# Performance work log

Measured on AMD Instinct MI355X. Metric: run time of the kernel, lower is better.

## Reference

```python
import jax, jax.numpy as jnp
import numpy as np

DIM = 1024


def setup_inputs() -> dict:
    key = jax.random.key(0)
    ks = jax.random.split(key, 10)
    B, S, D = 4, 2048, DIM
    std = 1.0 / np.sqrt(D)  # torch Linear default uniform bound
    return {
        "query": jax.random.normal(ks[0], (B, S, D), jnp.float32),
        "key": jax.random.normal(ks[1], (B, S, D), jnp.float32),
        "value": jax.random.normal(ks[2], (B, S, D), jnp.float32),
        "context": jnp.zeros((D,), jnp.float32),
        "Wq": jax.random.uniform(ks[3], (D, D), jnp.float32, -std, std),
        "bq": jax.random.uniform(ks[4], (D,), jnp.float32, -std, std),
        "Wk": jax.random.uniform(ks[5], (D, D), jnp.float32, -std, std),
        "bk": jax.random.uniform(ks[6], (D,), jnp.float32, -std, std),
        "Wv": jax.random.uniform(ks[7], (D, D), jnp.float32, -std, std),
        "bv": jax.random.uniform(ks[8], (D,), jnp.float32, -std, std),
    }


def reference(query, key, value, context, Wq, bq, Wk, bk, Wv, bv):
    scale = query.shape[-1] ** -0.5
    # torch Linear: x @ W.T + b
    q = (query + context) @ Wq.T + bq          # [B,S,D]
    k = (key + context) @ Wk.T + bk            # [B,S,D]
    v = value @ Wv.T + bv                      # [B,S,D]
    scores = jnp.einsum("bqd,bkd->bqk", q, k) * scale  # [B,S,S]
    weights = jax.nn.softmax(scores, axis=-1)
    return jnp.einsum("bqk,bkd->bqd", weights, v)
```

## Files before the change

kernel.cpp:

```cpp
#include <hip/hip_runtime.h>

typedef __attribute__((ext_vector_type(8))) short bf16x8;
typedef __attribute__((ext_vector_type(4))) float floatx4;

constexpr int BATCH = 4;
constexpr int SEQ   = 2048;
constexpr int DIMN  = 1024;
constexpr int M1    = BATCH * SEQ;

__device__ __forceinline__ short f2bf(float f) {
    union { float f; unsigned u; } x; x.f = f;
    unsigned r = x.u + 0x7fffu + ((x.u >> 16) & 1u);
    return (short)(r >> 16);
}
__device__ __forceinline__ float bf2f(short s) {
    union { unsigned u; float f; } x; x.u = ((unsigned)(unsigned short)s) << 16;
    return x.f;
}

__device__ __forceinline__ void async16(const void* g, void* l) {
    __builtin_amdgcn_global_load_lds(
        (const __attribute__((address_space(1))) unsigned int*)g,
        (__attribute__((address_space(3))) unsigned int*)l, 16, 0, 0);
}

#define WAITVM(N) asm volatile("s_waitcnt vmcnt(" #N ")" ::: "memory")
#define MEMFENCE  asm volatile("" ::: "memory")
#define BAR()     __builtin_amdgcn_s_barrier()
#define PRIO(x)   __builtin_amdgcn_s_setprio(x)

template<bool OUT_BF16, int WM>
__device__ __forceinline__ void gemm_core(
    const short* __restrict__ Ab, int lda,
    const short* __restrict__ Bb, int ldb,
    void* __restrict__ Cb, int ldc,
    const float* __restrict__ bias, int K, float scale,
    int m0, int n0)
{
    constexpr int ACH  = WM / 2;
    constexpr int ABY  = WM * 4096;
    constexpr int BUFB = ABY + 32768;
    __shared__ alignas(16) char smem[2][BUFB];
    char* lds = &smem[0][0];

    const int t    = threadIdx.x;
    const int lane = t & 63;
    const int wave = t >> 6;
    const int wr   = wave >> 2;
    const int wc   = wave & 3;
    const int lr   = lane & 15;
    const int lq   = lane >> 4;

    const int srow = t >> 3;
    const int scol = (((t & 7) * 16) ^ (((t >> 3) & 7) << 4)) >> 1;
    const short* pa = Ab + (size_t)(m0 + srow) * lda + scol;
    const short* pb = Bb + (size_t)(n0 + srow) * ldb + scol;
    const size_t rsa = (size_t)64 * lda;
    const size_t rsb = (size_t)64 * ldb;
    const int ldst = t * 16;

    const int roA0 = (wr * (WM * 16) + lr) * 128;
    const int roB0 = ABY + (wc * 64 + lr) * 128;
    const int cp0  = (lq << 4) ^ ((lane & 7) << 4);

    floatx4 acc[WM][4];
    #pragma unroll
    for (int m = 0; m < WM; ++m)
        #pragma unroll
        for (int n = 0; n < 4; ++n) acc[m][n] = (floatx4)(0.f);

    auto stA = [&](int dstb) {
        #pragma unroll
        for (int c = 0; c < ACH; ++c)
            async16(pa + (size_t)c * rsa, lds + dstb + c * 8192 + ldst);
        pa += 64;
    };
    auto stB01 = [&](int dstb) {
        async16(pb,       lds + dstb + ABY +        ldst);
        async16(pb + rsb, lds + dstb + ABY + 8192 + ldst);
    };
    auto stB23 = [&](int dstb) {
        async16(pb + 2 * rsb, lds + dstb + ABY + 16384 + ldst);
        async16(pb + 3 * rsb, lds + dstb + ABY + 24576 + ldst);
        pb += 64;
    };

    const int NT = K >> 6;

    stA(0); stB01(0); stB23(0); stA(BUFB);
    if constexpr (WM == 8) WAITVM(4); else WAITVM(2);
    BAR();

    for (int tt = 0; tt < NT; tt += 2) {
        #pragma unroll
        for (int half = 0; half < 2; ++half) {
            const int bufb = half ? BUFB : 0;
            const int tc   = tt + half;
            const char* rb = lds + bufb;

            if constexpr (WM == 8) {
                bf16x8 af[8], bq_[4];
                #pragma unroll
                for (int m = 0; m < 8; ++m)
                    af[m] = *(const bf16x8*)(rb + roA0 + m * 2048 + cp0);
                bq_[0] = *(const bf16x8*)(rb + roB0 +        cp0);
                bq_[1] = *(const bf16x8*)(rb + roB0 + 2048 + cp0);
                if (tc + 1 < NT) stB01(bufb ^ BUFB);
                BAR(); MEMFENCE;
                PRIO(1);
                #pragma unroll
                for (int m = 0; m < 8; ++m) {
                    acc[m][0] = __builtin_amdgcn_mfma_f32_16x16x32_bf16(af[m], bq_[0], acc[m][0], 0, 0, 0);
                    acc[m][1] = __builtin_amdgcn_mfma_f32_16x16x32_bf16(af[m], bq_[1], acc[m][1], 0, 0, 0);
                }
                PRIO(0);
                MEMFENCE; BAR();
                bq_[2] = *(const bf16x8*)(rb + roB0 + 2 * 2048 + cp0);
                bq_[3] = *(const bf16x8*)(rb + roB0 + 3 * 2048 + cp0);
                if (tc + 1 < NT) stB23(bufb ^ BUFB);
                BAR(); MEMFENCE;
                PRIO(1);
                #pragma unroll
                for (int m = 0; m < 8; ++m) {
                    acc[m][2] = __builtin_amdgcn_mfma_f32_16x16x32_bf16(af[m], bq_[2], acc[m][2], 0, 0, 0);
                    acc[m][3] = __builtin_amdgcn_mfma_f32_16x16x32_bf16(af[m], bq_[3], acc[m][3], 0, 0, 0);
                }
                PRIO(0);
                MEMFENCE; BAR();
                #pragma unroll
                for (int m = 0; m < 8; ++m)
                    af[m] = *(const bf16x8*)(rb + roA0 + m * 2048 + (cp0 ^ 64));
                bq_[0] = *(const bf16x8*)(rb + roB0 +        (cp0 ^ 64));
                bq_[1] = *(const bf16x8*)(rb + roB0 + 2048 + (cp0 ^ 64));
                BAR(); MEMFENCE;
                PRIO(1);
                #pragma unroll
                for (int m = 0; m < 8; ++m) {
                    acc[m][0] = __builtin_amdgcn_mfma_f32_16x16x32_bf16(af[m], bq_[0], acc[m][0], 0, 0, 0);
                    acc[m][1] = __builtin_amdgcn_mfma_f32_16x16x32_bf16(af[m], bq_[1], acc[m][1], 0, 0, 0);
                }
                PRIO(0);
                MEMFENCE; BAR();
                bq_[2] = *(const bf16x8*)(rb + roB0 + 2 * 2048 + (cp0 ^ 64));
                bq_[3] = *(const bf16x8*)(rb + roB0 + 3 * 2048 + (cp0 ^ 64));
                if (tc + 2 < NT) stA(bufb);
                BAR(); MEMFENCE;
                PRIO(1);
                #pragma unroll
                for (int m = 0; m < 8; ++m) {
                    acc[m][2] = __builtin_amdgcn_mfma_f32_16x16x32_bf16(af[m], bq_[2], acc[m][2], 0, 0, 0);
                    acc[m][3] = __builtin_amdgcn_mfma_f32_16x16x32_bf16(af[m], bq_[3], acc[m][3], 0, 0, 0);
                }
                PRIO(0);
                MEMFENCE;
                if (tc + 2 < NT)      { WAITVM(4); }
                else if (tc + 1 < NT) { WAITVM(0); }
                BAR();
            } else {
                bf16x8 af[4][2], bq_[2][2];
                #pragma unroll
                for (int m = 0; m < 4; ++m) {
                    af[m][0] = *(const bf16x8*)(rb + roA0 + m * 2048 + cp0);
                    af[m][1] = *(const bf16x8*)(rb + roA0 + m * 2048 + (cp0 ^ 64));
                }
                #pragma unroll
                for (int n = 0; n < 2; ++n) {
                    bq_[n][0] = *(const bf16x8*)(rb + roB0 + n * 2048 + cp0);
                    bq_[n][1] = *(const bf16x8*)(rb + roB0 + n * 2048 + (cp0 ^ 64));
                }
                if (tc + 1 < NT) { stB01(bufb ^ BUFB); stB23(bufb ^ BUFB); }
                BAR(); MEMFENCE;
                PRIO(1);
                #pragma unroll
                for (int m = 0; m < 4; ++m)
                    #pragma unroll
                    for (int n = 0; n < 2; ++n) {
                        acc[m][n] = __builtin_amdgcn_mfma_f32_16x16x32_bf16(af[m][0], bq_[n][0], acc[m][n], 0, 0, 0);
                        acc[m][n] = __builtin_amdgcn_mfma_f32_16x16x32_bf16(af[m][1], bq_[n][1], acc[m][n], 0, 0, 0);
                    }
                PRIO(0);
                MEMFENCE; BAR();
                #pragma unroll
                for (int n = 0; n < 2; ++n) {
                    bq_[n][0] = *(const bf16x8*)(rb + roB0 + (n + 2) * 2048 + cp0);
                    bq_[n][1] = *(const bf16x8*)(rb + roB0 + (n + 2) * 2048 + (cp0 ^ 64));
                }
                if (tc + 2 < NT) stA(bufb);
                BAR(); MEMFENCE;
                PRIO(1);
                #pragma unroll
                for (int m = 0; m < 4; ++m)
                    #pragma unroll
                    for (int n = 0; n < 2; ++n) {
                        acc[m][n + 2] = __builtin_amdgcn_mfma_f32_16x16x32_bf16(af[m][0], bq_[n][0], acc[m][n + 2], 0, 0, 0);
                        acc[m][n + 2] = __builtin_amdgcn_mfma_f32_16x16x32_bf16(af[m][1], bq_[n][1], acc[m][n + 2], 0, 0, 0);
                    }
                PRIO(0);
                MEMFENCE;
                if (tc + 2 < NT)      { WAITVM(2); }
                else if (tc + 1 < NT) { WAITVM(0); }
                BAR();
            }
        }
    }

    #pragma unroll
    for (int n = 0; n < 4; ++n) {
        const int gn = n0 + wc * 64 + n * 16 + lr;
        const float bv = bias ? bias[gn] : 0.f;
        #pragma unroll
        for (int m = 0; m < WM; ++m) {
            #pragma unroll
            for (int r = 0; r < 4; ++r) {
                const int gm = m0 + wr * (WM * 16) + m * 16 + lq * 4 + r;
                const float v = acc[m][n][r] * scale + bv;
                if (OUT_BF16) ((short*)Cb)[(size_t)gm * ldc + gn] = f2bf(v);
                else          ((float*)Cb)[(size_t)gm * ldc + gn] = v;
            }
        }
    }
}

__global__ __launch_bounds__(512, 2)
void proj_qkv(const short* __restrict__ xq, const short* __restrict__ xk,
              const short* __restrict__ xv,
              const short* __restrict__ Wq_, const short* __restrict__ Wk_,
              const short* __restrict__ Wv_,
              const float* __restrict__ bq_, const float* __restrict__ bk_,
              const float* __restrict__ bv_,
              short* __restrict__ q, short* __restrict__ k, short* __restrict__ vp)
{
    const int b   = blockIdx.x;
    const int xcd = b & 7;
    const int i   = b >> 3;
    const int z   = i >> 5;
    const int r   = i & 31;
    const int mm  = r >> 2;
    const int nn  = r & 3;
    const short* X = (z == 0) ? xq : (z == 1) ? xk : xv;
    const short* W = (z == 0) ? Wq_ : (z == 1) ? Wk_ : Wv_;
    const float* bb = (z == 0) ? bq_ : (z == 1) ? bk_ : bv_;
    short* O = (z == 0) ? q : (z == 1) ? k : vp;
    gemm_core<true, 4>(X, DIMN, W, DIMN, (void*)O, DIMN, bb, DIMN, 1.f,
                       (xcd * 8 + mm) * 128, nn * 256);
}

__global__ __launch_bounds__(512, 2)
void gemm_scores(const short* __restrict__ q, const short* __restrict__ k,
                 short* __restrict__ S, float scale)
{
    const int b   = blockIdx.x;
    const int xcd = b & 7;
    const int i   = b >> 3;
    const int bz  = xcd >> 1;
    const int mh  = xcd & 1;
    const int mm  = i >> 3;
    const int nn  = i & 7;
    gemm_core<true, 8>(q + (size_t)bz * SEQ * DIMN, DIMN,
                       k + (size_t)bz * SEQ * DIMN, DIMN,
                       (void*)(S + (size_t)bz * SEQ * SEQ), SEQ,
                       nullptr, DIMN, scale,
                       (mh * 4 + mm) * 256, nn * 256);
}

__global__ __launch_bounds__(512, 2)
void gemm_pv(const short* __restrict__ P, const short* __restrict__ vt,
             float* __restrict__ O)
{
    const int b   = blockIdx.x;
    const int xcd = b & 7;
    const int i   = b >> 3;
    const int bz  = xcd >> 1;
    const int mh  = xcd & 1;
    const int mm  = i >> 2;
    const int nn  = i & 3;
    gemm_core<false, 4>(P  + (size_t)bz * SEQ * SEQ,  SEQ,
                        vt + (size_t)bz * DIMN * SEQ, SEQ,
                        (void*)(O + (size_t)bz * SEQ * DIMN), DIMN,
                        nullptr, SEQ, 1.f,
                        (mh * 8 + mm) * 128, nn * 256);
}

__global__ __launch_bounds__(256)
void cvt_tri(const float* __restrict__ in0, short* __restrict__ out0,
             const float* __restrict__ in1, short* __restrict__ out1,
             const float* __restrict__ in2, short* __restrict__ out2, int n8)
{
    const int z = blockIdx.z;
    const float* in = (z == 0) ? in0 : (z == 1) ? in1 : in2;
    short* out      = (z == 0) ? out0 : (z == 1) ? out1 : out2;
    const int i = blockIdx.x * 256 + threadIdx.x;
    if (i >= n8) return;
    const float4 a0 = ((const float4*)in)[(size_t)i * 2];
    const float4 a1 = ((const float4*)in)[(size_t)i * 2 + 1];
    const float v[8] = {a0.x, a0.y, a0.z, a0.w, a1.x, a1.y, a1.z, a1.w};
    bf16x8 o;
    #pragma unroll
    for (int j = 0; j < 8; ++j) o[j] = f2bf(v[j]);
    *(bf16x8*)(out + (size_t)i * 8) = o;
}

__global__ __launch_bounds__(256)
void bias3(const float* __restrict__ Wq, const float* __restrict__ Wk,
           const float* __restrict__ Wv,
           const float* __restrict__ bq, const float* __restrict__ bk,
           const float* __restrict__ bv,
           const float* __restrict__ ctx,
           float* __restrict__ oq, float* __restrict__ ok, float* __restrict__ ov)
{
    const int z = blockIdx.y;
    const float* W = (z == 0) ? Wq : (z == 1) ? Wk : Wv;
    const float* b = (z == 0) ? bq : (z == 1) ? bk : bv;
    float*       o = (z == 0) ? oq : (z == 1) ? ok : ov;
    const int n    = blockIdx.x * 4 + (threadIdx.x >> 6);
    const int lane = threadIdx.x & 63;
    float s = 0.f;
    if (z < 2) {
        const float* row = W + (size_t)n * DIMN;
        for (int k = lane * 4; k < DIMN; k += 256) {
            const float4 x = *(const float4*)(row + k);
            const float4 c = *(const float4*)(ctx + k);
            s += x.x * c.x + x.y * c.y + x.z * c.z + x.w * c.w;
        }
        #pragma unroll
        for (int off = 32; off > 0; off >>= 1) s += __shfl_xor(s, off);
    }
    if (lane == 0) o[n] = b[n] + s;
}

__global__ __launch_bounds__(256)
void transpose_v(const short* __restrict__ in, short* __restrict__ out)
{
    __shared__ short t[64][68];
    const int b  = blockIdx.z;
    const int d0 = blockIdx.x * 64;
    const int s0 = blockIdx.y * 64;
    const int r  = threadIdx.x >> 3;
    const int c  = (threadIdx.x & 7) * 8;
    #pragma unroll
    for (int h = 0; h < 2; ++h) {
        const int s = r + h * 32;
        bf16x8 v = *(const bf16x8*)(in + ((size_t)b * SEQ + s0 + s) * DIMN + d0 + c);
        #pragma unroll
        for (int j = 0; j < 8; ++j) t[c + j][s] = v[j];
    }
    __syncthreads();
    #pragma unroll
    for (int h = 0; h < 2; ++h) {
        const int d = r + h * 32;
        bf16x8 v;
        #pragma unroll
        for (int j = 0; j < 8; ++j) v[j] = t[d][c + j];
        *(bf16x8*)(out + ((size_t)b * DIMN + d0 + d) * SEQ + s0 + c) = v;
    }
}

__global__ __launch_bounds__(256)
void softmax_kernel(short* __restrict__ P)
{
    const int bid = blockIdx.x;
    const int xcd = bid & 7;
    const int i   = bid >> 3;
    const int row = (xcd >> 1) * SEQ + (xcd & 1) * 1024 + i;
    short* p = P + (size_t)row * SEQ;
    const int t    = threadIdx.x;
    const int lane = t & 63;
    const int wave = t >> 6;
    __shared__ float red[8];

    bf16x8 raw = *(const bf16x8*)(p + t * 8);
    float v[8];
    float mx = -1e30f;
    #pragma unroll
    for (int j = 0; j < 8; ++j) { v[j] = bf2f(raw[j]); mx = fmaxf(mx, v[j]); }
    #pragma unroll
    for (int off = 32; off > 0; off >>= 1) mx = fmaxf(mx, __shfl_xor(mx, off));
    if (lane == 0) red[wave] = mx;
    __syncthreads();
    mx = fmaxf(fmaxf(red[0], red[1]), fmaxf(red[2], red[3]));

    float e[8], s = 0.f;
    #pragma unroll
    for (int j = 0; j < 8; ++j) { e[j] = __expf(v[j] - mx); s += e[j]; }
    #pragma unroll
    for (int off = 32; off > 0; off >>= 1) s += __shfl_xor(s, off);
    if (lane == 0) red[4 + wave] = s;
    __syncthreads();
    s = red[4] + red[5] + red[6] + red[7];
    const float inv = 1.f / s;

    bf16x8 o;
    #pragma unroll
    for (int j = 0; j < 8; ++j) o[j] = f2bf(e[j] * inv);
    *(bf16x8*)(p + t * 8) = o;
}

extern "C" void kernel_launch(void* const* d_in, const int* in_sizes, int n_in,
                              void* d_out, int out_size, void* d_ws, size_t ws_size,
                              hipStream_t stream)
{
    const float* query = (const float*)d_in[0];
    const float* key_  = (const float*)d_in[1];
    const float* value = (const float*)d_in[2];
    const float* ctx   = (const float*)d_in[3];
    const float* Wq    = (const float*)d_in[4];
    const float* bq    = (const float*)d_in[5];
    const float* Wk    = (const float*)d_in[6];
    const float* bk    = (const float*)d_in[7];
    const float* Wv    = (const float*)d_in[8];
    const float* bv    = (const float*)d_in[9];

    char* ws = (char*)d_ws;
    char* od = (char*)d_out;
    const size_t MB = 1ull << 20;
    short* xq   = (short*)(ws);
    short* xk   = (short*)(ws + 16 * MB);
    short* q_b  = (short*)(ws + 32 * MB);
    short* k_b  = (short*)(ws + 48 * MB);
    short* Wq_b = (short*)(ws + 64 * MB);
    short* Wk_b = (short*)(ws + 66 * MB);
    short* Wv_b = (short*)(ws + 68 * MB);
    float* bq_e = (float*)(ws + 70 * MB);
    float* bk_e = (float*)(ws + 70 * MB + 4096);
    float* bv_e = (float*)(ws + 70 * MB + 8192);
    short* S_b  = (short*)(ws);
    short* v_t  = (short*)(ws + 64 * MB);
    short* xv   = (short*)(od);
    short* vp   = (short*)(od + 16 * MB);

    dim3 blk(256);
    dim3 blk512(512);
    const int W8 = DIMN * DIMN / 8;
    const int X8 = M1 * DIMN / 8;

    cvt_tri<<<dim3(W8 / 256, 1, 3), blk, 0, stream>>>(Wq, Wq_b, Wk, Wk_b, Wv, Wv_b, W8);
    bias3<<<dim3(DIMN / 4, 3), blk, 0, stream>>>(Wq, Wk, Wv, bq, bk, bv, ctx,
                                                 bq_e, bk_e, bv_e);
    cvt_tri<<<dim3(X8 / 256, 1, 3), blk, 0, stream>>>(query, xq, key_, xk, value, xv, X8);

    proj_qkv<<<dim3(768), blk512, 0, stream>>>(xq, xk, xv, Wq_b, Wk_b, Wv_b,
                                               bq_e, bk_e, bv_e, q_b, k_b, vp);
    transpose_v<<<dim3(DIMN / 64, SEQ / 64, BATCH), blk, 0, stream>>>(vp, v_t);

    const float scale = 1.0f / 32.0f;
    gemm_scores<<<dim3(256), blk512, 0, stream>>>(q_b, k_b, S_b, scale);

    softmax_kernel<<<dim3(M1), blk, 0, stream>>>(S_b);

    gemm_pv<<<dim3(256), blk512, 0, stream>>>(S_b, v_t, (float*)d_out);
}
```

Measured before the change: 304.3 us.

## Fuse fp32-to-bf16 input conversion into projection GEMM and restructure score GEMM pipeline

Drops the separate cvt_tri pass over query/key/value. The projection GEMM now loads fp32 activations into registers, converts them to bf16 and writes them into swizzled LDS itself, which removes a full read-write round trip of three 32 MB inputs. The scores GEMM gets a new four-phase single-tile loop that stages A and B in quarters across the MFMA phases. The PV GEMM is split out into its own simplified core. The risk is more register pressure and VALU conversion work inside the projection mainloop, plus a different overlap pattern in the scores kernel.

```diff
diff --git a/kernel.cpp b/kernel.cpp
--- a/kernel.cpp
+++ b/kernel.cpp
@@ -1,6 +1,7 @@
 #include <hip/hip_runtime.h>
 
 typedef __attribute__((ext_vector_type(8))) short bf16x8;
+typedef __attribute__((ext_vector_type(4))) short short4v;
 typedef __attribute__((ext_vector_type(4))) float floatx4;
 
 constexpr int BATCH = 4;
@@ -25,23 +26,21 @@
 }
 
 #define WAITVM(N) asm volatile("s_waitcnt vmcnt(" #N ")" ::: "memory")
-#define MEMFENCE  asm volatile("" ::: "memory")
+#define LGKM0     asm volatile("s_waitcnt lgkmcnt(0)" ::: "memory")
 #define BAR()     __builtin_amdgcn_s_barrier()
 #define PRIO(x)   __builtin_amdgcn_s_setprio(x)
 
-template<bool OUT_BF16, int WM>
-__device__ __forceinline__ void gemm_core(
+template<bool OUT_BF16>
+__device__ __forceinline__ void gemm4ph(
     const short* __restrict__ Ab, int lda,
     const short* __restrict__ Bb, int ldb,
     void* __restrict__ Cb, int ldc,
     const float* __restrict__ bias, int K, float scale,
     int m0, int n0)
 {
-    constexpr int ACH  = WM / 2;
-    constexpr int ABY  = WM * 4096;
-    constexpr int BUFB = ABY + 32768;
-    __shared__ alignas(16) char smem[2][BUFB];
-    char* lds = &smem[0][0];
+    constexpr int BUFB = 65536;
+    __shared__ alignas(16) char smem[2 * BUFB];
+    char* lds = smem;
 
     const int t    = threadIdx.x;
     const int lane = t & 63;
@@ -51,6 +50,306 @@
     const int lr   = lane & 15;
     const int lq   = lane >> 4;
 
+    const int srow  = t >> 3;
+    const int scolB = ((t & 7) * 16) ^ ((srow & 7) << 4);
+    const short* pa = Ab + (size_t)(m0 + srow) * lda + (scolB >> 1);
+    const short* pb = Bb + (size_t)(n0 + srow) * ldb + (scolB >> 1);
+    const size_t rsa = (size_t)64 * lda;
+    const size_t rsb = (size_t)64 * ldb;
+    const int ldst = t * 16;
+
+    const int roA = (wr * 128 + lr) * 128;
+    const int roB = 32768 + (wc * 64 + lr) * 128;
+    const int cs  = (lane & 7) << 4;
+    const int cp0 = (lq << 4) ^ cs;
+    const int cp1 = (64 | (lq << 4)) ^ cs;
+
+    floatx4 acc[8][4];
+    #pragma unroll
+    for (int m = 0; m < 8; ++m)
+        #pragma unroll
+        for (int n = 0; n < 4; ++n) acc[m][n] = (floatx4)(0.f);
+
+    auto stA01 = [&](int d) {
+        async16(pa,       lds + d +        ldst);
+        async16(pa + rsa, lds + d + 8192 + ldst);
+    };
+    auto stA23 = [&](int d) {
+        async16(pa + 2 * rsa, lds + d + 16384 + ldst);
+        async16(pa + 3 * rsa, lds + d + 24576 + ldst);
+        pa += 64;
+    };
+    auto stB01 = [&](int d) {
+        async16(pb,       lds + d + 32768 + ldst);
+        async16(pb + rsb, lds + d + 40960 + ldst);
+    };
+    auto stB23 = [&](int d) {
+        async16(pb + 2 * rsb, lds + d + 49152 + ldst);
+        async16(pb + 3 * rsb, lds + d + 57344 + ldst);
+        pb += 64;
+    };
+
+    const int NT = K >> 6;
+
+    stA01(0); stA23(0); stB01(0); stB23(0);
+    WAITVM(0);
+    BAR();
+
+    int bu = 0;
+    for (int tt = 0; tt < NT; ++tt) {
+        const bool stg = tt + 1 < NT;
+        const int  ob  = bu ^ BUFB;
+        const char* rb = lds + bu;
+        bf16x8 af[4], bq_[4];
+
+        if (stg) stA01(ob);
+        #pragma unroll
+        for (int m = 0; m < 4; ++m) af[m]  = *(const bf16x8*)(rb + roA + m * 2048 + cp0);
+        #pragma unroll
+        for (int n = 0; n < 4; ++n) bq_[n] = *(const bf16x8*)(rb + roB + n * 2048 + cp0);
+        BAR();
+        PRIO(1);
+        #pragma unroll
+        for (int m = 0; m < 4; ++m)
+            #pragma unroll
+            for (int n = 0; n < 4; ++n)
+                acc[m][n] = __builtin_amdgcn_mfma_f32_16x16x32_bf16(af[m], bq_[n], acc[m][n], 0, 0, 0);
+        PRIO(0);
+        BAR();
+
+        if (stg) stA23(ob);
+        #pragma unroll
+        for (int m = 0; m < 4; ++m) af[m] = *(const bf16x8*)(rb + roA + (m + 4) * 2048 + cp0);
+        BAR();
+        PRIO(1);
+        #pragma unroll
+        for (int m = 0; m < 4; ++m)
+            #pragma unroll
+            for (int n = 0; n < 4; ++n)
+                acc[m + 4][n] = __builtin_amdgcn_mfma_f32_16x16x32_bf16(af[m], bq_[n], acc[m + 4][n], 0, 0, 0);
+        PRIO(0);
+        BAR();
+
+        if (stg) stB01(ob);
+        #pragma unroll
+        for (int m = 0; m < 4; ++m) af[m]  = *(const bf16x8*)(rb + roA + m * 2048 + cp1);
+        #pragma unroll
+        for (int n = 0; n < 4; ++n) bq_[n] = *(const bf16x8*)(rb + roB + n * 2048 + cp1);
+        BAR();
+        PRIO(1);
+        #pragma unroll
+        for (int m = 0; m < 4; ++m)
+            #pragma unroll
+            for (int n = 0; n < 4; ++n)
+                acc[m][n] = __builtin_amdgcn_mfma_f32_16x16x32_bf16(af[m], bq_[n], acc[m][n], 0, 0, 0);
+        PRIO(0);
+        BAR();
+
+        if (stg) stB23(ob);
+        #pragma unroll
+        for (int m = 0; m < 4; ++m) af[m] = *(const bf16x8*)(rb + roA + (m + 4) * 2048 + cp1);
+        BAR();
+        PRIO(1);
+        #pragma unroll
+        for (int m = 0; m < 4; ++m)
+            #pragma unroll
+            for (int n = 0; n < 4; ++n)
+                acc[m + 4][n] = __builtin_amdgcn_mfma_f32_16x16x32_bf16(af[m], bq_[n], acc[m + 4][n], 0, 0, 0);
+        PRIO(0);
+        WAITVM(0);
+        BAR();
+        bu = ob;
+    }
+
+    #pragma unroll
+    for (int n = 0; n < 4; ++n) {
+        const int gn = n0 + wc * 64 + n * 16 + lr;
+        const float bv = bias ? bias[gn] : 0.f;
+        #pragma unroll
+        for (int m = 0; m < 8; ++m) {
+            #pragma unroll
+            for (int r = 0; r < 4; ++r) {
+                const int gm = m0 + wr * 128 + m * 16 + lq * 4 + r;
+                const float v = acc[m][n][r] * scale + bv;
+                if (OUT_BF16) ((short*)Cb)[(size_t)gm * ldc + gn] = f2bf(v);
+                else          ((float*)Cb)[(size_t)gm * ldc + gn] = v;
+            }
+        }
+    }
+}
+
+__device__ __forceinline__ void proj_core(
+    const float* __restrict__ Af, int lda,
+    const short* __restrict__ Bb, int ldb,
+    short* __restrict__ Cb, int ldc,
+    const float* __restrict__ bias, int K,
+    int m0, int n0)
+{
+    constexpr int ABY  = 16384;
+    constexpr int BUFB = ABY + 32768;
+    __shared__ alignas(16) char smem[2 * BUFB];
+    char* lds = smem;
+
+    const int t    = threadIdx.x;
+    const int lane = t & 63;
+    const int wave = t >> 6;
+    const int wr   = wave >> 2;
+    const int wc   = wave & 3;
+    const int lr   = lane & 15;
+    const int lq   = lane >> 4;
+
+    const int srow  = t >> 3;
+    const int scolB = ((t & 7) * 16) ^ ((srow & 7) << 4);
+    const short* pb = Bb + (size_t)(n0 + srow) * ldb + (scolB >> 1);
+    const size_t rsb = (size_t)64 * ldb;
+    const int ldst = t * 16;
+
+    const float* pafb = Af + (size_t)(m0 + (t >> 4)) * lda + (t & 15) * 4;
+    const size_t opstr = (size_t)32 * lda;
+    int dwA[4];
+    #pragma unroll
+    for (int o = 0; o < 4; ++o) {
+        const int row = o * 32 + (t >> 4);
+        dwA[o] = row * 128 + (((t & 15) * 8) ^ ((row & 7) << 4));
+    }
+
+    const int roA = (wr * 64 + lr) * 128;
+    const int roB = ABY + (wc * 64 + lr) * 128;
+    const int cs  = (lane & 7) << 4;
+    const int cp0 = (lq << 4) ^ cs;
+    const int cp1 = (64 | (lq << 4)) ^ cs;
+
+    floatx4 acc[4][4];
+    #pragma unroll
+    for (int m = 0; m < 4; ++m)
+        #pragma unroll
+        for (int n = 0; n < 4; ++n) acc[m][n] = (floatx4)(0.f);
+
+    auto stB01 = [&](int d) {
+        async16(pb,       lds + d + ABY +        ldst);
+        async16(pb + rsb, lds + d + ABY + 8192 + ldst);
+    };
+    auto stB23 = [&](int d) {
+        async16(pb + 2 * rsb, lds + d + ABY + 16384 + ldst);
+        async16(pb + 3 * rsb, lds + d + ABY + 24576 + ldst);
+        pb += 64;
+    };
+    float4 rA[4];
+    auto loadA = [&]() {
+        #pragma unroll
+        for (int o = 0; o < 4; ++o)
+            rA[o] = *(const float4*)(pafb + (size_t)o * opstr);
+        pafb += 64;
+    };
+    auto writeA = [&](int d) {
+        #pragma unroll
+        for (int o = 0; o < 4; ++o) {
+            short4v pk;
+            pk[0] = f2bf(rA[o].x); pk[1] = f2bf(rA[o].y);
+            pk[2] = f2bf(rA[o].z); pk[3] = f2bf(rA[o].w);
+            *(short4v*)(lds + d + dwA[o]) = pk;
+        }
+    };
+
+    const int NT = K >> 6;
+
+    loadA();
+    stB01(0); stB23(0);
+    WAITVM(4);
+    writeA(0);
+    LGKM0;
+    WAITVM(0);
+    BAR();
+
+    int bu = 0;
+    for (int tt = 0; tt < NT; ++tt) {
+        const bool stg = tt + 1 < NT;
+        const int  ob  = bu ^ BUFB;
+        const char* rb = lds + bu;
+        bf16x8 af[4][2], bq_[2][2];
+
+        if (stg) { loadA(); stB01(ob); stB23(ob); }
+        #pragma unroll
+        for (int m = 0; m < 4; ++m) {
+            af[m][0] = *(const bf16x8*)(rb + roA + m * 2048 + cp0);
+            af[m][1] = *(const bf16x8*)(rb + roA + m * 2048 + cp1);
+        }
+        #pragma unroll
+        for (int n = 0; n < 2; ++n) {
+            bq_[n][0] = *(const bf16x8*)(rb + roB + n * 2048 + cp0);
+            bq_[n][1] = *(const bf16x8*)(rb + roB + n * 2048 + cp1);
+        }
+        BAR();
+        PRIO(1);
+        #pragma unroll
+        for (int m = 0; m < 4; ++m)
+            #pragma unroll
+            for (int n = 0; n < 2; ++n) {
+                acc[m][n] = __builtin_amdgcn_mfma_f32_16x16x32_bf16(af[m][0], bq_[n][0], acc[m][n], 0, 0, 0);
+                acc[m][n] = __builtin_amdgcn_mfma_f32_16x16x32_bf16(af[m][1], bq_[n][1], acc[m][n], 0, 0, 0);
+            }
+        PRIO(0);
+        BAR();
+
+        #pragma unroll
+        for (int n = 0; n < 2; ++n) {
+            bq_[n][0] = *(const bf16x8*)(rb + roB + (n + 2) * 2048 + cp0);
+            bq_[n][1] = *(const bf16x8*)(rb + roB + (n + 2) * 2048 + cp1);
+        }
+        if (stg) {
+            WAITVM(4);
+            writeA(ob);
+        }
+        BAR();
+        PRIO(1);
+        #pragma unroll
+        for (int m = 0; m < 4; ++m)
+            #pragma unroll
+            for (int n = 0; n < 2; ++n) {
+                acc[m][n + 2] = __builtin_amdgcn_mfma_f32_16x16x32_bf16(af[m][0], bq_[n][0], acc[m][n + 2], 0, 0, 0);
+                acc[m][n + 2] = __builtin_amdgcn_mfma_f32_16x16x32_bf16(af[m][1], bq_[n][1], acc[m][n + 2], 0, 0, 0);
+            }
+        PRIO(0);
+        LGKM0;
+        WAITVM(0);
+        BAR();
+        bu = ob;
+    }
+
+    #pragma unroll
+    for (int n = 0; n < 4; ++n) {
+        const int gn = n0 + wc * 64 + n * 16 + lr;
+        const float bv = bias[gn];
+        #pragma unroll
+        for (int m = 0; m < 4; ++m) {
+            #pragma unroll
+            for (int r = 0; r < 4; ++r) {
+                const int gm = m0 + wr * 64 + m * 16 + lq * 4 + r;
+                Cb[(size_t)gm * ldc + gn] = f2bf(acc[m][n][r] + bv);
+            }
+        }
+    }
+}
+
+__device__ __forceinline__ void gemm_pv_core(
+    const short* __restrict__ Ab, int lda,
+    const short* __restrict__ Bb, int ldb,
+    float* __restrict__ Cb, int ldc, int K,
+    int m0, int n0)
+{
+    constexpr int ABY  = 16384;
+    constexpr int BUFB = ABY + 32768;
+    __shared__ alignas(16) char smem[2][BUFB];
+    char* lds = &smem[0][0];
+
+    const int t    = threadIdx.x;
+    const int lane = t & 63;
+    const int wave = t >> 6;
+    const int wr   = wave >> 2;
+    const int wc   = wave & 3;
+    const int lr   = lane & 15;
+    const int lq   = lane >> 4;
+
     const int srow = t >> 3;
     const int scol = (((t & 7) * 16) ^ (((t >> 3) & 7) << 4)) >> 1;
     const short* pa = Ab + (size_t)(m0 + srow) * lda + scol;
@@ -59,20 +358,19 @@
     const size_t rsb = (size_t)64 * ldb;
     const int ldst = t * 16;
 
-    const int roA0 = (wr * (WM * 16) + lr) * 128;
+    const int roA0 = (wr * 64 + lr) * 128;
     const int roB0 = ABY + (wc * 64 + lr) * 128;
     const int cp0  = (lq << 4) ^ ((lane & 7) << 4);
 
-    floatx4 acc[WM][4];
-    #pragma unroll
-    for (int m = 0; m < WM; ++m)
+    floatx4 acc[4][4];
+    #pragma unroll
+    for (int m = 0; m < 4; ++m)
         #pragma unroll
         for (int n = 0; n < 4; ++n) acc[m][n] = (floatx4)(0.f);
 
     auto stA = [&](int dstb) {
-        #pragma unroll
-        for (int c = 0; c < ACH; ++c)
-            async16(pa + (size_t)c * rsa, lds + dstb + c * 8192 + ldst);
+        async16(pa,       lds + dstb +        ldst);
+        async16(pa + rsa, lds + dstb + 8192 + ldst);
         pa += 64;
     };
     auto stB01 = [&](int dstb) {
@@ -86,144 +384,75 @@
     };
 
     const int NT = K >> 6;
-
     stA(0); stB01(0); stB23(0); stA(BUFB);
-    if constexpr (WM == 8) WAITVM(4); else WAITVM(2);
+    WAITVM(2);
     BAR();
 
-    for (int tt = 0; tt < NT; tt += 2) {
-        #pragma unroll
-        for (int half = 0; half < 2; ++half) {
-            const int bufb = half ? BUFB : 0;
-            const int tc   = tt + half;
-            const char* rb = lds + bufb;
-
-            if constexpr (WM == 8) {
-                bf16x8 af[8], bq_[4];
-                #pragma unroll
-                for (int m = 0; m < 8; ++m)
-                    af[m] = *(const bf16x8*)(rb + roA0 + m * 2048 + cp0);
-                bq_[0] = *(const bf16x8*)(rb + roB0 +        cp0);
-                bq_[1] = *(const bf16x8*)(rb + roB0 + 2048 + cp0);
-                if (tc + 1 < NT) stB01(bufb ^ BUFB);
-                BAR(); MEMFENCE;
-                PRIO(1);
-                #pragma unroll
-                for (int m = 0; m < 8; ++m) {
-                    acc[m][0] = __builtin_amdgcn_mfma_f32_16x16x32_bf16(af[m], bq_[0], acc[m][0], 0, 0, 0);
-                    acc[m][1] = __builtin_amdgcn_mfma_f32_16x16x32_bf16(af[m], bq_[1], acc[m][1], 0, 0, 0);
-                }
-                PRIO(0);
-                MEMFENCE; BAR();
-                bq_[2] = *(const bf16x8*)(rb + roB0 + 2 * 2048 + cp0);
-                bq_[3] = *(const bf16x8*)(rb + roB0 + 3 * 2048 + cp0);
-                if (tc + 1 < NT) stB23(bufb ^ BUFB);
-                BAR(); MEMFENCE;
-                PRIO(1);
-                #pragma unroll
-                for (int m = 0; m < 8; ++m) {
-                    acc[m][2] = __builtin_amdgcn_mfma_f32_16x16x32_bf16(af[m], bq_[2], acc[m][2], 0, 0, 0);
-                    acc[m][3] = __builtin_amdgcn_mfma_f32_16x16x32_bf16(af[m], bq_[3], acc[m][3], 0, 0, 0);
-                }
-                PRIO(0);
-                MEMFENCE; BAR();
-                #pragma unroll
-                for (int m = 0; m < 8; ++m)
-                    af[m] = *(const bf16x8*)(rb + roA0 + m * 2048 + (cp0 ^ 64));
-                bq_[0] = *(const bf16x8*)(rb + roB0 +        (cp0 ^ 64));
-                bq_[1] = *(const bf16x8*)(rb + roB0 + 2048 + (cp0 ^ 64));
-                BAR(); MEMFENCE;
-                PRIO(1);
-                #pragma unroll
-                for (int m = 0; m < 8; ++m) {
-                    acc[m][0] = __builtin_amdgcn_mfma_f32_16x16x32_bf16(af[m], bq_[0], acc[m][0], 0, 0, 0);
-                    acc[m][1] = __builtin_amdgcn_mfma_f32_16x16x32_bf16(af[m], bq_[1], acc[m][1], 0, 0, 0);
-                }
-                PRIO(0);
-                MEMFENCE; BAR();
-                bq_[2] = *(const bf16x8*)(rb + roB0 + 2 * 2048 + (cp0 ^ 64));
-                bq_[3] = *(const bf16x8*)(rb + roB0 + 3 * 2048 + (cp0 ^ 64));
-                if (tc + 2 < NT) stA(bufb);
-                BAR(); MEMFENCE;
-                PRIO(1);
-                #pragma unroll
-                for (int m = 0; m < 8; ++m) {
-                    acc[m][2] = __builtin_amdgcn_mfma_f32_16x16x32_bf16(af[m], bq_[2], acc[m][2], 0, 0, 0);
-                    acc[m][3] = __builtin_amdgcn_mfma_f32_16x16x32_bf16(af[m], bq_[3], acc[m][3], 0, 0, 0);
-                }
-                PRIO(0);
-                MEMFENCE;
-                if (tc + 2 < NT)      { WAITVM(4); }
-                else if (tc + 1 < NT) { WAITVM(0); }
-                BAR();
-            } else {
-                bf16x8 af[4][2], bq_[2][2];
-                #pragma unroll
-                for (int m = 0; m < 4; ++m) {
-                    af[m][0] = *(const bf16x8*)(rb + roA0 + m * 2048 + cp0);
-                    af[m][1] = *(const bf16x8*)(rb + roA0 + m * 2048 + (cp0 ^ 64));
-                }
-                #pragma unroll
-                for (int n = 0; n < 2; ++n) {
-                    bq_[n][0] = *(const bf16x8*)(rb + roB0 + n * 2048 + cp0);
-                    bq_[n][1] = *(const bf16x8*)(rb + roB0 + n * 2048 + (cp0 ^ 64));
-                }
-                if (tc + 1 < NT) { stB01(bufb ^ BUFB); stB23(bufb ^ BUFB); }
-                BAR(); MEMFENCE;
-                PRIO(1);
-                #pragma unroll
-                for (int m = 0; m < 4; ++m)
-                    #pragma unroll
-                    for (int n = 0; n < 2; ++n) {
-                        acc[m][n] = __builtin_amdgcn_mfma_f32_16x16x32_bf16(af[m][0], bq_[n][0], acc[m][n], 0, 0, 0);
-                        acc[m][n] = __builtin_amdgcn_mfma_f32_16x16x32_bf16(af[m][1], bq_[n][1], acc[m][n], 0, 0, 0);
-                    }
-                PRIO(0);
-                MEMFENCE; BAR();
-                #pragma unroll
-                for (int n = 0; n < 2; ++n) {
-                    bq_[n][0] = *(const bf16x8*)(rb + roB0 + (n + 2) * 2048 + cp0);
-                    bq_[n][1] = *(const bf16x8*)(rb + roB0 + (n + 2) * 2048 + (cp0 ^ 64));
-                }
-                if (tc + 2 < NT) stA(bufb);
-                BAR(); MEMFENCE;
-                PRIO(1);
-                #pragma unroll
-                for (int m = 0; m < 4; ++m)
-                    #pragma unroll
-                    for (int n = 0; n < 2; ++n) {
-                        acc[m][n + 2] = __builtin_amdgcn_mfma_f32_16x16x32_bf16(af[m][0], bq_[n][0], acc[m][n + 2], 0, 0, 0);
-                        acc[m][n + 2] = __builtin_amdgcn_mfma_f32_16x16x32_bf16(af[m][1], bq_[n][1], acc[m][n + 2], 0, 0, 0);
-                    }
-                PRIO(0);
-                MEMFENCE;
-                if (tc + 2 < NT)      { WAITVM(2); }
-                else if (tc + 1 < NT) { WAITVM(0); }
-                BAR();
+    int bufb = 0;
+    for (int tc = 0; tc < NT; ++tc) {
+        const char* rb = lds + bufb;
+        bf16x8 af[4][2], bq_[2][2];
+        #pragma unroll
+        for (int m = 0; m < 4; ++m) {
+            af[m][0] = *(const bf16x8*)(rb + roA0 + m * 2048 + cp0);
+            af[m][1] = *(const bf16x8*)(rb + roA0 + m * 2048 + (cp0 ^ 64));
+        }
+        #pragma unroll
+        for (int n = 0; n < 2; ++n) {
+            bq_[n][0] = *(const bf16x8*)(rb + roB0 + n * 2048 + cp0);
+            bq_[n][1] = *(const bf16x8*)(rb + roB0 + n * 2048 + (cp0 ^ 64));
+        }
+        if (tc + 1 < NT) { stB01(bufb ^ BUFB); stB23(bufb ^ BUFB); }
+        BAR();
+        PRIO(1);
+        #pragma unroll
+        for (int m = 0; m < 4; ++m)
+            #pragma unroll
+            for (int n = 0; n < 2; ++n) {
+                acc[m][n] = __builtin_amdgcn_mfma_f32_16x16x32_bf16(af[m][0], bq_[n][0], acc[m][n], 0, 0, 0);
+                acc[m][n] = __builtin_amdgcn_mfma_f32_16x16x32_bf16(af[m][1], bq_[n][1], acc[m][n], 0, 0, 0);
             }
-        }
+        PRIO(0);
+        BAR();
+        #pragma unroll
+        for (int n = 0; n < 2; ++n) {
+            bq_[n][0] = *(const bf16x8*)(rb + roB0 + (n + 2) * 2048 + cp0);
+            bq_[n][1] = *(const bf16x8*)(rb + roB0 + (n + 2) * 2048 + (cp0 ^ 64));
+        }
+        if (tc + 2 < NT) stA(bufb);
+        BAR();
+        PRIO(1);
+        #pragma unroll
+        for (int m = 0; m < 4; ++m)
+            #pragma unroll
+            for (int n = 0; n < 2; ++n) {
+                acc[m][n + 2] = __builtin_amdgcn_mfma_f32_16x16x32_bf16(af[m][0], bq_[n][0], acc[m][n + 2], 0, 0, 0);
+                acc[m][n + 2] = __builtin_amdgcn_mfma_f32_16x16x32_bf16(af[m][1], bq_[n][1], acc[m][n + 2], 0, 0, 0);
+            }
+        PRIO(0);
+        if (tc + 2 < NT)      { WAITVM(2); }
+        else if (tc + 1 < NT) { WAITVM(0); }
+        BAR();
+        bufb ^= BUFB;
     }
 
     #pragma unroll
     for (int n = 0; n < 4; ++n) {
         const int gn = n0 + wc * 64 + n * 16 + lr;
-        const float bv = bias ? bias[gn] : 0.f;
-        #pragma unroll
-        for (int m = 0; m < WM; ++m) {
+        #pragma unroll
+        for (int m = 0; m < 4; ++m) {
             #pragma unroll
             for (int r = 0; r < 4; ++r) {
-                const int gm = m0 + wr * (WM * 16) + m * 16 + lq * 4 + r;
-                const float v = acc[m][n][r] * scale + bv;
-                if (OUT_BF16) ((short*)Cb)[(size_t)gm * ldc + gn] = f2bf(v);
-                else          ((float*)Cb)[(size_t)gm * ldc + gn] = v;
+                const int gm = m0 + wr * 64 + m * 16 + lq * 4 + r;
+                Cb[(size_t)gm * ldc + gn] = acc[m][n][r];
             }
         }
     }
 }
 
 __global__ __launch_bounds__(512, 2)
-void proj_qkv(const short* __restrict__ xq, const short* __restrict__ xk,
-              const short* __restrict__ xv,
+void proj_qkv(const float* __restrict__ xq, const float* __restrict__ xk,
+              const float* __restrict__ xv,
               const short* __restrict__ Wq_, const short* __restrict__ Wk_,
               const short* __restrict__ Wv_,
               const float* __restrict__ bq_, const float* __restrict__ bk_,
@@ -237,12 +466,12 @@
     const int r   = i & 31;
     const int mm  = r >> 2;
     const int nn  = r & 3;
-    const short* X = (z == 0) ? xq : (z == 1) ? xk : xv;
+    const float* X = (z == 0) ? xq : (z == 1) ? xk : xv;
     const short* W = (z == 0) ? Wq_ : (z == 1) ? Wk_ : Wv_;
     const float* bb = (z == 0) ? bq_ : (z == 1) ? bk_ : bv_;
     short* O = (z == 0) ? q : (z == 1) ? k : vp;
-    gemm_core<true, 4>(X, DIMN, W, DIMN, (void*)O, DIMN, bb, DIMN, 1.f,
-                       (xcd * 8 + mm) * 128, nn * 256);
+    proj_core(X, DIMN, W, DIMN, O, DIMN, bb, DIMN,
+              (xcd * 8 + mm) * 128, nn * 256);
 }
 
 __global__ __launch_bounds__(512, 2)
@@ -256,11 +485,11 @@
     const int mh  = xcd & 1;
     const int mm  = i >> 3;
     const int nn  = i & 7;
-    gemm_core<true, 8>(q + (size_t)bz * SEQ * DIMN, DIMN,
-                       k + (size_t)bz * SEQ * DIMN, DIMN,
-                       (void*)(S + (size_t)bz * SEQ * SEQ), SEQ,
-                       nullptr, DIMN, scale,
-                       (mh * 4 + mm) * 256, nn * 256);
+    gemm4ph<true>(q + (size_t)bz * SEQ * DIMN, DIMN,
+                  k + (size_t)bz * SEQ * DIMN, DIMN,
+                  (void*)(S + (size_t)bz * SEQ * SEQ), SEQ,
+                  nullptr, DIMN, scale,
+                  (mh * 4 + mm) * 256, nn * 256);
 }
 
 __global__ __launch_bounds__(512, 2)
@@ -274,11 +503,10 @@
     const int mh  = xcd & 1;
     const int mm  = i >> 2;
     const int nn  = i & 3;
-    gemm_core<false, 4>(P  + (size_t)bz * SEQ * SEQ,  SEQ,
-                        vt + (size_t)bz * DIMN * SEQ, SEQ,
-                        (void*)(O + (size_t)bz * SEQ * DIMN), DIMN,
-                        nullptr, SEQ, 1.f,
-                        (mh * 8 + mm) * 128, nn * 256);
+    gemm_pv_core(P  + (size_t)bz * SEQ * SEQ,  SEQ,
+                 vt + (size_t)bz * DIMN * SEQ, SEQ,
+                 O + (size_t)bz * SEQ * DIMN, DIMN, SEQ,
+                 (mh * 8 + mm) * 128, nn * 256);
 }
 
 __global__ __launch_bounds__(256)
@@ -411,10 +639,8 @@
     const float* bv    = (const float*)d_in[9];
 
     char* ws = (char*)d_ws;
-    char* od = (char*)d_out;
     const size_t MB = 1ull << 20;
-    short* xq   = (short*)(ws);
-    short* xk   = (short*)(ws + 16 * MB);
+    short* vp   = (short*)(ws);
     short* q_b  = (short*)(ws + 32 * MB);
     short* k_b  = (short*)(ws + 48 * MB);
     short* Wq_b = (short*)(ws + 64 * MB);
@@ -425,20 +651,17 @@
     float* bv_e = (float*)(ws + 70 * MB + 8192);
     short* S_b  = (short*)(ws);
     short* v_t  = (short*)(ws + 64 * MB);
-    short* xv   = (short*)(od);
-    short* vp   = (short*)(od + 16 * MB);
 
     dim3 blk(256);
     dim3 blk512(512);
     const int W8 = DIMN * DIMN / 8;
-    const int X8 = M1 * DIMN / 8;
 
     cvt_tri<<<dim3(W8 / 256, 1, 3), blk, 0, stream>>>(Wq, Wq_b, Wk, Wk_b, Wv, Wv_b, W8);
     bias3<<<dim3(DIMN / 4, 3), blk, 0, stream>>>(Wq, Wk, Wv, bq, bk, bv, ctx,
                                                  bq_e, bk_e, bv_e);
-    cvt_tri<<<dim3(X8 / 256, 1, 3), blk, 0, stream>>>(query, xq, key_, xk, value, xv, X8);
-
-    proj_qkv<<<dim3(768), blk512, 0, stream>>>(xq, xk, xv, Wq_b, Wk_b, Wv_b,
+
+    proj_qkv<<<dim3(768), blk512, 0, stream>>>(query, key_, value,
+                                               Wq_b, Wk_b, Wv_b,
                                                bq_e, bk_e, bv_e, q_b, k_b, vp);
     transpose_v<<<dim3(DIMN / 64, SEQ / 64, BATCH), blk, 0, stream>>>(vp, v_t);
 
```

New measurement: 328.6 us. 8.0% more time.
